# Kernel tuning notes

Hardware: AMD Instinct MI355X
Metric: run time of the kernel (lower is better)

Reference implementation:

```python
import jax, jax.numpy as jnp
import numpy as np

B, S, HID = 1, 2048, 4096
NH, NKV, HD = 32, 8, 128          # num_heads, num_key_value_heads, head_dim
N_REP = NH // NKV                  # GQA group size
ROPE_BASE = 10000.0


def rotate_half(x):
    x1, x2 = jnp.split(x, 2, axis=-1)
    return jnp.concatenate([-x2, x1], axis=-1)


def setup_inputs() -> dict:
    key = jax.random.key(0)
    k_hs, k_q, k_k, k_v, k_o = jax.random.split(key, 5)
    hidden_states = jax.random.normal(k_hs, (B, S, HID), dtype=jnp.float32)
    scale = 0.02
    wq = jax.random.normal(k_q, (HID, NH * HD), dtype=jnp.float32) * scale
    wk = jax.random.normal(k_k, (HID, NKV * HD), dtype=jnp.float32) * scale
    wv = jax.random.normal(k_v, (HID, NKV * HD), dtype=jnp.float32) * scale
    wo = jax.random.normal(k_o, (NH * HD, HID), dtype=jnp.float32) * scale
    # additive causal mask, 0 on/below diagonal, large negative above
    causal = jnp.tril(jnp.ones((S, S), dtype=bool))
    attention_mask = jnp.where(causal, 0.0, -1e9).astype(jnp.float32)[None, None]
    # RoPE cos/sin cache (LlamaRotaryEmbedding)
    inv_freq = 1.0 / (ROPE_BASE ** (jnp.arange(0, HD, 2, dtype=jnp.float32) / HD))
    t = jnp.arange(S, dtype=jnp.float32)
    freqs = jnp.outer(t, inv_freq)                 # [S, HD/2]
    emb = jnp.concatenate([freqs, freqs], axis=-1)  # [S, HD]
    cos, sin = jnp.cos(emb), jnp.sin(emb)
    return {"hidden_states": hidden_states, "attention_mask": attention_mask,
            "wq": wq, "wk": wk, "wv": wv, "wo": wo, "cos": cos, "sin": sin}


def reference(hidden_states, attention_mask, wq, wk, wv, wo, cos, sin):
    b, s, _ = hidden_states.shape
    # projections -> [b, heads, s, head_dim]
    q = (hidden_states @ wq).reshape(b, s, NH, HD).transpose(0, 2, 1, 3)
    k = (hidden_states @ wk).reshape(b, s, NKV, HD).transpose(0, 2, 1, 3)
    v = (hidden_states @ wv).reshape(b, s, NKV, HD).transpose(0, 2, 1, 3)
    # RoPE: cos/sin [s, hd] broadcast over batch and heads
    c = cos[None, None, :, :]
    sn = sin[None, None, :, :]
    q = q * c + rotate_half(q) * sn
    k = k * c + rotate_half(k) * sn
    # GQA repeat_kv: [b, nkv, s, d] -> [b, nh, s, d]
    k = jnp.repeat(k, N_REP, axis=1)
    v = jnp.repeat(v, N_REP, axis=1)
    scores = jnp.einsum('bhqd,bhkd->bhqk', q, k) / jnp.sqrt(jnp.float32(HD))
    scores = scores + attention_mask
    attn = jax.nn.softmax(scores.astype(jnp.float32), axis=-1).astype(q.dtype)
    out = jnp.einsum('bhqk,bhkd->bhqd', attn, v)        # [b, nh, s, d]
    out = out.transpose(0, 2, 1, 3).reshape(b, s, NH * HD)
    return out @ wo
```

## Files before the change

### kernel.cpp

```cpp
#include <hip/hip_runtime.h>


typedef __bf16 bf16_t;
typedef bf16_t bf16x8_t __attribute__((ext_vector_type(8)));
typedef float f32x4_t __attribute__((ext_vector_type(4)));

#define S_LEN 2048
#define HID 4096
#define NH 32
#define NKV 8
#define HD 128
#define KV_DIM 1024
#define QKV_DIM 6144
#define SCALE 0.08838834764831845f

__device__ __align__(16) bf16_t g_hsb[(size_t)S_LEN * HID];
__device__ __align__(16) bf16_t g_wqkvT[(size_t)QKV_DIM * HID];
__device__ __align__(16) bf16_t g_woT[(size_t)HID * HID];
__device__ __align__(16) bf16_t g_qkv[(size_t)S_LEN * QKV_DIM];
__device__ __align__(16) bf16_t g_vT[(size_t)NKV * HD * S_LEN];
__device__ __align__(16) bf16_t g_ao[(size_t)S_LEN * HID];

__device__ __forceinline__ void gl_lds16(const bf16_t* g, bf16_t* l) {
  __builtin_amdgcn_global_load_lds(
      (const __attribute__((address_space(1))) void*)g,
      (__attribute__((address_space(3))) void*)l, 16, 0, 0);
}

__global__ __launch_bounds__(256) void cast_f32_bf16(
    const float* __restrict__ in, bf16_t* __restrict__ out)
{
  size_t i = ((size_t)blockIdx.x * 256 + threadIdx.x) * 8;
  float4 a = *(const float4*)(in + i);
  float4 b = *(const float4*)(in + i + 4);
  bf16x8_t r;
  r[0] = (bf16_t)a.x; r[1] = (bf16_t)a.y; r[2] = (bf16_t)a.z; r[3] = (bf16_t)a.w;
  r[4] = (bf16_t)b.x; r[5] = (bf16_t)b.y; r[6] = (bf16_t)b.z; r[7] = (bf16_t)b.w;
  *(bf16x8_t*)(out + i) = r;
}

__global__ __launch_bounds__(256) void transpose_f32_bf16(
    const float* __restrict__ in, bf16_t* __restrict__ out, int is, int os)
{
  __shared__ __align__(16) bf16_t T[64 * 72];
  int r0 = blockIdx.x * 64, c0 = blockIdx.y * 64;
  int t = threadIdx.x;
#pragma unroll
  for (int it = 0; it < 2; ++it) {
    int idx = t + it * 256;
    int r = idx >> 3, c8 = (idx & 7) * 8;
    const float* p = in + (size_t)(r0 + r) * is + c0 + c8;
    float4 a = *(const float4*)p;
    float4 b = *(const float4*)(p + 4);
    bf16x8_t x;
    x[0] = (bf16_t)a.x; x[1] = (bf16_t)a.y; x[2] = (bf16_t)a.z; x[3] = (bf16_t)a.w;
    x[4] = (bf16_t)b.x; x[5] = (bf16_t)b.y; x[6] = (bf16_t)b.z; x[7] = (bf16_t)b.w;
    *(bf16x8_t*)(T + r * 72 + c8) = x;
  }
  __syncthreads();
#pragma unroll
  for (int it = 0; it < 2; ++it) {
    int idx = t + it * 256;
    int c = idx >> 3, r8 = (idx & 7) * 8;
    bf16x8_t x;
#pragma unroll
    for (int i = 0; i < 8; ++i) x[i] = T[(r8 + i) * 72 + c];
    *(bf16x8_t*)(out + (size_t)(c0 + c) * os + r0 + r8) = x;
  }
}

__global__ __launch_bounds__(256) void transpose_bf16(
    const bf16_t* __restrict__ in, bf16_t* __restrict__ out,
    int is, int os, int in_b, int out_b)
{
  __shared__ __align__(16) bf16_t T[64 * 72];
  const bf16_t* inp = in + (size_t)blockIdx.z * in_b;
  bf16_t* outp = out + (size_t)blockIdx.z * out_b;
  int r0 = blockIdx.x * 64, c0 = blockIdx.y * 64;
  int t = threadIdx.x;
#pragma unroll
  for (int it = 0; it < 2; ++it) {
    int idx = t + it * 256;
    int r = idx >> 3, c8 = (idx & 7) * 8;
    *(bf16x8_t*)(T + r * 72 + c8) =
        *(const bf16x8_t*)(inp + (size_t)(r0 + r) * is + c0 + c8);
  }
  __syncthreads();
#pragma unroll
  for (int it = 0; it < 2; ++it) {
    int idx = t + it * 256;
    int c = idx >> 3, r8 = (idx & 7) * 8;
    bf16x8_t x;
#pragma unroll
    for (int i = 0; i < 8; ++i) x[i] = T[(r8 + i) * 72 + c];
    *(bf16x8_t*)(outp + (size_t)(c0 + c) * os + r0 + r8) = x;
  }
}

template <typename CT>
__global__ __launch_bounds__(256) void gemm128(
    const bf16_t* __restrict__ A, const bf16_t* __restrict__ Bt,
    CT* __restrict__ C, int K, int N)
{
  __shared__ __align__(16) bf16_t As[128 * 32];
  __shared__ __align__(16) bf16_t Bs[128 * 32];
  int t = threadIdx.x;
  int wave = t >> 6, lane = t & 63, ln = lane & 15, lq = lane >> 4;
  int m0 = blockIdx.x * 128, n0 = blockIdx.y * 128;
  int wm = (wave >> 1) * 64, wn = (wave & 1) * 64;
  int srow = wave * 16 + (lane >> 2);
  int skc = (lane & 3) * 8;
  const bf16_t* Ag0 = A + (size_t)(m0 + srow) * K + skc;
  const bf16_t* Ag1 = A + (size_t)(m0 + 64 + srow) * K + skc;
  const bf16_t* Bg0 = Bt + (size_t)(n0 + srow) * K + skc;
  const bf16_t* Bg1 = Bt + (size_t)(n0 + 64 + srow) * K + skc;
  bf16_t* Al0 = As + (wave * 16) * 32;
  bf16_t* Al1 = As + (64 + wave * 16) * 32;
  bf16_t* Bl0 = Bs + (wave * 16) * 32;
  bf16_t* Bl1 = Bs + (64 + wave * 16) * 32;
  f32x4_t acc[4][4] = {};
  for (int k0 = 0; k0 < K; k0 += 32) {
    __syncthreads();
    gl_lds16(Ag0 + k0, Al0);
    gl_lds16(Ag1 + k0, Al1);
    gl_lds16(Bg0 + k0, Bl0);
    gl_lds16(Bg1 + k0, Bl1);
    __syncthreads();
    bf16x8_t af[4], bfr[4];
#pragma unroll
    for (int i = 0; i < 4; ++i) {
      af[i]  = *(const bf16x8_t*)(As + (wm + i * 16 + ln) * 32 + lq * 8);
      bfr[i] = *(const bf16x8_t*)(Bs + (wn + i * 16 + ln) * 32 + lq * 8);
    }
#pragma unroll
    for (int mt = 0; mt < 4; ++mt)
#pragma unroll
      for (int nt = 0; nt < 4; ++nt)
        acc[mt][nt] = __builtin_amdgcn_mfma_f32_16x16x32_bf16(
            af[mt], bfr[nt], acc[mt][nt], 0, 0, 0);
  }
#pragma unroll
  for (int mt = 0; mt < 4; ++mt)
#pragma unroll
    for (int nt = 0; nt < 4; ++nt)
#pragma unroll
      for (int r = 0; r < 4; ++r)
        C[(size_t)(m0 + wm + mt * 16 + lq * 4 + r) * N + n0 + wn + nt * 16 + ln] =
            (CT)acc[mt][nt][r];
}

__global__ __launch_bounds__(256) void rope_kernel(
    bf16_t* __restrict__ qkv, const float* __restrict__ cs,
    const float* __restrict__ sn)
{
  int idx = blockIdx.x * 256 + threadIdx.x;
  int d = idx & 63;
  int h = (idx >> 6) % (NH + NKV);
  int s = idx / (64 * (NH + NKV));
  float c = cs[s * HD + d], si = sn[s * HD + d];
  bf16_t* base = qkv + (size_t)s * QKV_DIM +
                 ((h < NH) ? h * HD : HID + (h - NH) * HD);
  float x1 = (float)base[d], x2 = (float)base[d + 64];
  base[d]      = (bf16_t)(x1 * c - x2 * si);
  base[d + 64] = (bf16_t)(x2 * c + x1 * si);
}

__global__ __launch_bounds__(256) void attn_kernel(
    const bf16_t* __restrict__ QKV, const bf16_t* __restrict__ VT,
    bf16_t* __restrict__ O)
{
  __shared__ __align__(16) bf16_t Ks[64 * 136];
  __shared__ __align__(16) bf16_t Vs[128 * 72];
  __shared__ __align__(16) bf16_t Ps[4 * 16 * 72];
  int t = threadIdx.x, wave = t >> 6, lane = t & 63;
  int ln = lane & 15, lq = lane >> 4;
  int bid = blockIdx.x;
  int qb = (S_LEN / 64 - 1) - (bid >> 5);
  int head = bid & 31, kvh = head >> 2;
  int q0 = qb * 64;
  int qr = q0 + wave * 16 + ln;

  bf16x8_t qf[4];
#pragma unroll
  for (int kk = 0; kk < 4; ++kk)
    qf[kk] = *(const bf16x8_t*)(QKV + (size_t)qr * QKV_DIM + head * HD +
                                kk * 32 + lq * 8);

  f32x4_t oa[8] = {};
  float m_r[4] = {-1e30f, -1e30f, -1e30f, -1e30f};
  float l_r[4] = {0.f, 0.f, 0.f, 0.f};

  int krow = t >> 4, kdc = (t & 15) * 8;
  int vrow = t >> 3, vkc = (t & 7) * 8;
  const bf16_t* Kg = QKV + HID + (size_t)kvh * HD;
  const bf16_t* Vg = VT + (size_t)kvh * HD * S_LEN;

  for (int kt = 0; kt <= qb; ++kt) {
    int kb = kt * 64;
    __syncthreads();
#pragma unroll
    for (int p = 0; p < 4; ++p) {
      int r_ = p * 16 + krow;
      *(bf16x8_t*)(Ks + r_ * 136 + kdc) =
          *(const bf16x8_t*)(Kg + (size_t)(kb + r_) * QKV_DIM + kdc);
      int d_ = p * 32 + vrow;
      *(bf16x8_t*)(Vs + d_ * 72 + vkc) =
          *(const bf16x8_t*)(Vg + (size_t)d_ * S_LEN + kb + vkc);
    }
    __syncthreads();

    f32x4_t sv[4] = {};
#pragma unroll
    for (int nt = 0; nt < 4; ++nt)
#pragma unroll
      for (int kk = 0; kk < 4; ++kk) {
        bf16x8_t kf = *(const bf16x8_t*)(Ks + (nt * 16 + ln) * 136 +
                                         kk * 32 + lq * 8);
        sv[nt] = __builtin_amdgcn_mfma_f32_16x16x32_bf16(qf[kk], kf, sv[nt],
                                                         0, 0, 0);
      }

    float p_[4][4];
    if (kt == qb) {
#pragma unroll
      for (int nt = 0; nt < 4; ++nt)
#pragma unroll
        for (int r = 0; r < 4; ++r) {
          int rq = wave * 16 + lq * 4 + r;
          p_[nt][r] = (nt * 16 + ln <= rq) ? sv[nt][r] * SCALE : -1e30f;
        }
    } else {
#pragma unroll
      for (int nt = 0; nt < 4; ++nt)
#pragma unroll
        for (int r = 0; r < 4; ++r) p_[nt][r] = sv[nt][r] * SCALE;
    }

    float mx[4];
#pragma unroll
    for (int r = 0; r < 4; ++r)
      mx[r] = fmaxf(fmaxf(p_[0][r], p_[1][r]), fmaxf(p_[2][r], p_[3][r]));
#pragma unroll
    for (int off = 8; off >= 1; off >>= 1)
#pragma unroll
      for (int r = 0; r < 4; ++r) mx[r] = fmaxf(mx[r], __shfl_xor(mx[r], off, 64));

    float al[4], rs[4];
#pragma unroll
    for (int r = 0; r < 4; ++r) {
      float mn = fmaxf(m_r[r], mx[r]);
      al[r] = __expf(m_r[r] - mn);
      m_r[r] = mn;
      rs[r] = 0.f;
#pragma unroll
      for (int nt = 0; nt < 4; ++nt) {
        p_[nt][r] = __expf(p_[nt][r] - mn);
        rs[r] += p_[nt][r];
      }
    }
#pragma unroll
    for (int off = 8; off >= 1; off >>= 1)
#pragma unroll
      for (int r = 0; r < 4; ++r) rs[r] += __shfl_xor(rs[r], off, 64);
#pragma unroll
    for (int r = 0; r < 4; ++r) l_r[r] = l_r[r] * al[r] + rs[r];
#pragma unroll
    for (int dt = 0; dt < 8; ++dt)
#pragma unroll
      for (int r = 0; r < 4; ++r) oa[dt][r] *= al[r];

    bf16_t* myP = Ps + wave * 16 * 72;
#pragma unroll
    for (int nt = 0; nt < 4; ++nt)
#pragma unroll
      for (int r = 0; r < 4; ++r)
        myP[(lq * 4 + r) * 72 + nt * 16 + ln] = (bf16_t)p_[nt][r];
    bf16x8_t pf0 = *(const bf16x8_t*)(myP + ln * 72 + lq * 8);
    bf16x8_t pf1 = *(const bf16x8_t*)(myP + ln * 72 + 32 + lq * 8);
#pragma unroll
    for (int dt = 0; dt < 8; ++dt) {
      bf16x8_t v0 = *(const bf16x8_t*)(Vs + (dt * 16 + ln) * 72 + lq * 8);
      bf16x8_t v1 = *(const bf16x8_t*)(Vs + (dt * 16 + ln) * 72 + 32 + lq * 8);
      oa[dt] = __builtin_amdgcn_mfma_f32_16x16x32_bf16(pf0, v0, oa[dt], 0, 0, 0);
      oa[dt] = __builtin_amdgcn_mfma_f32_16x16x32_bf16(pf1, v1, oa[dt], 0, 0, 0);
    }
  }

#pragma unroll
  for (int dt = 0; dt < 8; ++dt)
#pragma unroll
    for (int r = 0; r < 4; ++r) {
      int row = q0 + wave * 16 + lq * 4 + r;
      O[(size_t)row * HID + head * HD + dt * 16 + ln] =
          (bf16_t)(oa[dt][r] / l_r[r]);
    }
}

extern "C" void kernel_launch(void* const* d_in, const int* in_sizes, int n_in,
                              void* d_out, int out_size, void* d_ws, size_t ws_size,
                              hipStream_t stream)
{
  (void)in_sizes; (void)n_in; (void)out_size; (void)d_ws; (void)ws_size;
  const float* hs = (const float*)d_in[0];
  const float* wq = (const float*)d_in[2];
  const float* wk = (const float*)d_in[3];
  const float* wv = (const float*)d_in[4];
  const float* wo = (const float*)d_in[5];
  const float* cs = (const float*)d_in[6];
  const float* sn = (const float*)d_in[7];
  float* out = (float*)d_out;

  bf16_t *hsb, *wqkvT, *woT, *qkv, *vT, *ao;
  hipGetSymbolAddress((void**)&hsb,   HIP_SYMBOL(g_hsb));
  hipGetSymbolAddress((void**)&wqkvT, HIP_SYMBOL(g_wqkvT));
  hipGetSymbolAddress((void**)&woT,   HIP_SYMBOL(g_woT));
  hipGetSymbolAddress((void**)&qkv,   HIP_SYMBOL(g_qkv));
  hipGetSymbolAddress((void**)&vT,    HIP_SYMBOL(g_vT));
  hipGetSymbolAddress((void**)&ao,    HIP_SYMBOL(g_ao));

  cast_f32_bf16<<<(S_LEN * HID) / (256 * 8), 256, 0, stream>>>(hs, hsb);

  transpose_f32_bf16<<<dim3(64, 64), 256, 0, stream>>>(wq, wqkvT, HID, HID);
  transpose_f32_bf16<<<dim3(64, 16), 256, 0, stream>>>(
      wk, wqkvT + (size_t)HID * HID, KV_DIM, HID);
  transpose_f32_bf16<<<dim3(64, 16), 256, 0, stream>>>(
      wv, wqkvT + (size_t)(HID + KV_DIM) * HID, KV_DIM, HID);
  transpose_f32_bf16<<<dim3(64, 64), 256, 0, stream>>>(wo, woT, HID, HID);

  gemm128<bf16_t><<<dim3(S_LEN / 128, QKV_DIM / 128), 256, 0, stream>>>(
      hsb, wqkvT, qkv, HID, QKV_DIM);

  rope_kernel<<<(S_LEN * (NH + NKV) * 64) / 256, 256, 0, stream>>>(qkv, cs, sn);

  transpose_bf16<<<dim3(S_LEN / 64, HD / 64, NKV), 256, 0, stream>>>(
      qkv + HID + KV_DIM, vT, QKV_DIM, S_LEN, HD, HD * S_LEN);

  attn_kernel<<<dim3((S_LEN / 64) * NH), 256, 0, stream>>>(qkv, vT, ao);

  gemm128<float><<<dim3(S_LEN / 128, HID / 128), 256, 0, stream>>>(
      ao, woT, out, HID, HID);
}
```

Baseline: 673.6 us.

## Enlarge attention query tile to 128 rows per block, flatten GEMM grid

The attention kernel now handles 128 query rows per block, two 16-row tiles per wave, so each K/V tile loaded into shared memory serves twice as many queries. This halves K/V reload traffic and the number of barriers per unit of work, at the cost of more registers per thread and half as many blocks. Causal masking is applied to the last two key tiles. The GEMM launches also switch to a 1D grid with explicit m/n decoding, which keeps the same block order (m fastest).

```diff
diff --git a/kernel.cpp b/kernel.cpp
--- a/kernel.cpp
+++ b/kernel.cpp
@@ -100,13 +100,14 @@
 template <typename CT>
 __global__ __launch_bounds__(256) void gemm128(
     const bf16_t* __restrict__ A, const bf16_t* __restrict__ Bt,
-    CT* __restrict__ C, int K, int N)
+    CT* __restrict__ C, int K, int N, int MB)
 {
   __shared__ __align__(16) bf16_t As[128 * 32];
   __shared__ __align__(16) bf16_t Bs[128 * 32];
   int t = threadIdx.x;
   int wave = t >> 6, lane = t & 63, ln = lane & 15, lq = lane >> 4;
-  int m0 = blockIdx.x * 128, n0 = blockIdx.y * 128;
+  int id = blockIdx.x;
+  int m0 = (id % MB) * 128, n0 = (id / MB) * 128;
   int wm = (wave >> 1) * 64, wn = (wave & 1) * 64;
   int srow = wave * 16 + (lane >> 2);
   int skc = (lane & 3) * 8;
@@ -171,31 +172,37 @@
 {
   __shared__ __align__(16) bf16_t Ks[64 * 136];
   __shared__ __align__(16) bf16_t Vs[128 * 72];
-  __shared__ __align__(16) bf16_t Ps[4 * 16 * 72];
+  __shared__ __align__(16) bf16_t Ps[4 * 32 * 72];
   int t = threadIdx.x, wave = t >> 6, lane = t & 63;
   int ln = lane & 15, lq = lane >> 4;
   int bid = blockIdx.x;
-  int qb = (S_LEN / 64 - 1) - (bid >> 5);
+  int qblk = (S_LEN / 128 - 1) - (bid >> 5);
   int head = bid & 31, kvh = head >> 2;
-  int q0 = qb * 64;
-  int qr = q0 + wave * 16 + ln;
-
-  bf16x8_t qf[4];
-#pragma unroll
-  for (int kk = 0; kk < 4; ++kk)
-    qf[kk] = *(const bf16x8_t*)(QKV + (size_t)qr * QKV_DIM + head * HD +
-                                kk * 32 + lq * 8);
-
-  f32x4_t oa[8] = {};
-  float m_r[4] = {-1e30f, -1e30f, -1e30f, -1e30f};
-  float l_r[4] = {0.f, 0.f, 0.f, 0.f};
+  int q0 = qblk * 128;
+
+  bf16x8_t qf[2][4];
+#pragma unroll
+  for (int rt = 0; rt < 2; ++rt)
+#pragma unroll
+    for (int kk = 0; kk < 4; ++kk)
+      qf[rt][kk] = *(const bf16x8_t*)(
+          QKV + (size_t)(q0 + wave * 32 + rt * 16 + ln) * QKV_DIM +
+          head * HD + kk * 32 + lq * 8);
+
+  f32x4_t oa[2][8] = {};
+  float m_r[2][4], l_r[2][4];
+#pragma unroll
+  for (int rt = 0; rt < 2; ++rt)
+#pragma unroll
+    for (int r = 0; r < 4; ++r) { m_r[rt][r] = -1e30f; l_r[rt][r] = 0.f; }
 
   int krow = t >> 4, kdc = (t & 15) * 8;
   int vrow = t >> 3, vkc = (t & 7) * 8;
   const bf16_t* Kg = QKV + HID + (size_t)kvh * HD;
   const bf16_t* Vg = VT + (size_t)kvh * HD * S_LEN;
 
-  for (int kt = 0; kt <= qb; ++kt) {
+  int ktend = 2 * qblk + 1;
+  for (int kt = 0; kt <= ktend; ++kt) {
     int kb = kt * 64;
     __syncthreads();
 #pragma unroll
@@ -209,91 +216,114 @@
     }
     __syncthreads();
 
-    f32x4_t sv[4] = {};
+    f32x4_t sv[2][4] = {};
 #pragma unroll
     for (int nt = 0; nt < 4; ++nt)
 #pragma unroll
       for (int kk = 0; kk < 4; ++kk) {
         bf16x8_t kf = *(const bf16x8_t*)(Ks + (nt * 16 + ln) * 136 +
                                          kk * 32 + lq * 8);
-        sv[nt] = __builtin_amdgcn_mfma_f32_16x16x32_bf16(qf[kk], kf, sv[nt],
-                                                         0, 0, 0);
+        sv[0][nt] = __builtin_amdgcn_mfma_f32_16x16x32_bf16(qf[0][kk], kf,
+                                                            sv[0][nt], 0, 0, 0);
+        sv[1][nt] = __builtin_amdgcn_mfma_f32_16x16x32_bf16(qf[1][kk], kf,
+                                                            sv[1][nt], 0, 0, 0);
       }
 
-    float p_[4][4];
-    if (kt == qb) {
+    float p_[2][4][4];
+    if (kt >= 2 * qblk) {
+#pragma unroll
+      for (int rt = 0; rt < 2; ++rt)
+#pragma unroll
+        for (int nt = 0; nt < 4; ++nt)
+#pragma unroll
+          for (int r = 0; r < 4; ++r) {
+            int rowg = q0 + wave * 32 + rt * 16 + lq * 4 + r;
+            int colg = kb + nt * 16 + ln;
+            p_[rt][nt][r] = (colg <= rowg) ? sv[rt][nt][r] * SCALE : -1e30f;
+          }
+    } else {
+#pragma unroll
+      for (int rt = 0; rt < 2; ++rt)
+#pragma unroll
+        for (int nt = 0; nt < 4; ++nt)
+#pragma unroll
+          for (int r = 0; r < 4; ++r) p_[rt][nt][r] = sv[rt][nt][r] * SCALE;
+    }
+
+#pragma unroll
+    for (int rt = 0; rt < 2; ++rt) {
+      float mx[4], al[4], rs[4];
+#pragma unroll
+      for (int r = 0; r < 4; ++r)
+        mx[r] = fmaxf(fmaxf(p_[rt][0][r], p_[rt][1][r]),
+                      fmaxf(p_[rt][2][r], p_[rt][3][r]));
+#pragma unroll
+      for (int off = 8; off >= 1; off >>= 1)
+#pragma unroll
+        for (int r = 0; r < 4; ++r)
+          mx[r] = fmaxf(mx[r], __shfl_xor(mx[r], off, 64));
+#pragma unroll
+      for (int r = 0; r < 4; ++r) {
+        float mn = fmaxf(m_r[rt][r], mx[r]);
+        al[r] = __expf(m_r[rt][r] - mn);
+        m_r[rt][r] = mn;
+        rs[r] = 0.f;
+#pragma unroll
+        for (int nt = 0; nt < 4; ++nt) {
+          p_[rt][nt][r] = __expf(p_[rt][nt][r] - mn);
+          rs[r] += p_[rt][nt][r];
+        }
+      }
+#pragma unroll
+      for (int off = 8; off >= 1; off >>= 1)
+#pragma unroll
+        for (int r = 0; r < 4; ++r) rs[r] += __shfl_xor(rs[r], off, 64);
+#pragma unroll
+      for (int r = 0; r < 4; ++r) l_r[rt][r] = l_r[rt][r] * al[r] + rs[r];
+#pragma unroll
+      for (int dt = 0; dt < 8; ++dt)
+#pragma unroll
+        for (int r = 0; r < 4; ++r) oa[rt][dt][r] *= al[r];
+    }
+
+    bf16_t* myP = Ps + wave * 32 * 72;
+#pragma unroll
+    for (int rt = 0; rt < 2; ++rt)
 #pragma unroll
       for (int nt = 0; nt < 4; ++nt)
 #pragma unroll
-        for (int r = 0; r < 4; ++r) {
-          int rq = wave * 16 + lq * 4 + r;
-          p_[nt][r] = (nt * 16 + ln <= rq) ? sv[nt][r] * SCALE : -1e30f;
-        }
-    } else {
-#pragma unroll
-      for (int nt = 0; nt < 4; ++nt)
-#pragma unroll
-        for (int r = 0; r < 4; ++r) p_[nt][r] = sv[nt][r] * SCALE;
-    }
-
-    float mx[4];
-#pragma unroll
-    for (int r = 0; r < 4; ++r)
-      mx[r] = fmaxf(fmaxf(p_[0][r], p_[1][r]), fmaxf(p_[2][r], p_[3][r]));
-#pragma unroll
-    for (int off = 8; off >= 1; off >>= 1)
-#pragma unroll
-      for (int r = 0; r < 4; ++r) mx[r] = fmaxf(mx[r], __shfl_xor(mx[r], off, 64));
-
-    float al[4], rs[4];
-#pragma unroll
-    for (int r = 0; r < 4; ++r) {
-      float mn = fmaxf(m_r[r], mx[r]);
-      al[r] = __expf(m_r[r] - mn);
-      m_r[r] = mn;
-      rs[r] = 0.f;
-#pragma unroll
-      for (int nt = 0; nt < 4; ++nt) {
-        p_[nt][r] = __expf(p_[nt][r] - mn);
-        rs[r] += p_[nt][r];
-      }
-    }
-#pragma unroll
-    for (int off = 8; off >= 1; off >>= 1)
-#pragma unroll
-      for (int r = 0; r < 4; ++r) rs[r] += __shfl_xor(rs[r], off, 64);
-#pragma unroll
-    for (int r = 0; r < 4; ++r) l_r[r] = l_r[r] * al[r] + rs[r];
-#pragma unroll
-    for (int dt = 0; dt < 8; ++dt)
-#pragma unroll
-      for (int r = 0; r < 4; ++r) oa[dt][r] *= al[r];
-
-    bf16_t* myP = Ps + wave * 16 * 72;
-#pragma unroll
-    for (int nt = 0; nt < 4; ++nt)
-#pragma unroll
-      for (int r = 0; r < 4; ++r)
-        myP[(lq * 4 + r) * 72 + nt * 16 + ln] = (bf16_t)p_[nt][r];
-    bf16x8_t pf0 = *(const bf16x8_t*)(myP + ln * 72 + lq * 8);
-    bf16x8_t pf1 = *(const bf16x8_t*)(myP + ln * 72 + 32 + lq * 8);
+        for (int r = 0; r < 4; ++r)
+          myP[(rt * 16 + lq * 4 + r) * 72 + nt * 16 + ln] = (bf16_t)p_[rt][nt][r];
+    bf16x8_t pf[2][2];
+#pragma unroll
+    for (int rt = 0; rt < 2; ++rt) {
+      pf[rt][0] = *(const bf16x8_t*)(myP + (rt * 16 + ln) * 72 + lq * 8);
+      pf[rt][1] = *(const bf16x8_t*)(myP + (rt * 16 + ln) * 72 + 32 + lq * 8);
+    }
 #pragma unroll
     for (int dt = 0; dt < 8; ++dt) {
       bf16x8_t v0 = *(const bf16x8_t*)(Vs + (dt * 16 + ln) * 72 + lq * 8);
       bf16x8_t v1 = *(const bf16x8_t*)(Vs + (dt * 16 + ln) * 72 + 32 + lq * 8);
-      oa[dt] = __builtin_amdgcn_mfma_f32_16x16x32_bf16(pf0, v0, oa[dt], 0, 0, 0);
-      oa[dt] = __builtin_amdgcn_mfma_f32_16x16x32_bf16(pf1, v1, oa[dt], 0, 0, 0);
-    }
-  }
-
-#pragma unroll
-  for (int dt = 0; dt < 8; ++dt)
-#pragma unroll
-    for (int r = 0; r < 4; ++r) {
-      int row = q0 + wave * 16 + lq * 4 + r;
-      O[(size_t)row * HID + head * HD + dt * 16 + ln] =
-          (bf16_t)(oa[dt][r] / l_r[r]);
-    }
+#pragma unroll
+      for (int rt = 0; rt < 2; ++rt) {
+        oa[rt][dt] = __builtin_amdgcn_mfma_f32_16x16x32_bf16(pf[rt][0], v0,
+                                                             oa[rt][dt], 0, 0, 0);
+        oa[rt][dt] = __builtin_amdgcn_mfma_f32_16x16x32_bf16(pf[rt][1], v1,
+                                                             oa[rt][dt], 0, 0, 0);
+      }
+    }
+  }
+
+#pragma unroll
+  for (int rt = 0; rt < 2; ++rt)
+#pragma unroll
+    for (int dt = 0; dt < 8; ++dt)
+#pragma unroll
+      for (int r = 0; r < 4; ++r) {
+        int row = q0 + wave * 32 + rt * 16 + lq * 4 + r;
+        O[(size_t)row * HID + head * HD + dt * 16 + ln] =
+            (bf16_t)(oa[rt][dt][r] / l_r[rt][r]);
+      }
 }
 
 extern "C" void kernel_launch(void* const* d_in, const int* in_sizes, int n_in,
@@ -327,16 +357,16 @@
       wv, wqkvT + (size_t)(HID + KV_DIM) * HID, KV_DIM, HID);
   transpose_f32_bf16<<<dim3(64, 64), 256, 0, stream>>>(wo, woT, HID, HID);
 
-  gemm128<bf16_t><<<dim3(S_LEN / 128, QKV_DIM / 128), 256, 0, stream>>>(
-      hsb, wqkvT, qkv, HID, QKV_DIM);
+  gemm128<bf16_t><<<dim3((S_LEN / 128) * (QKV_DIM / 128)), 256, 0, stream>>>(
+      hsb, wqkvT, qkv, HID, QKV_DIM, S_LEN / 128);
 
   rope_kernel<<<(S_LEN * (NH + NKV) * 64) / 256, 256, 0, stream>>>(qkv, cs, sn);
 
   transpose_bf16<<<dim3(S_LEN / 64, HD / 64, NKV), 256, 0, stream>>>(
       qkv + HID + KV_DIM, vT, QKV_DIM, S_LEN, HD, HD * S_LEN);
 
-  attn_kernel<<<dim3((S_LEN / 64) * NH), 256, 0, stream>>>(qkv, vT, ao);
-
-  gemm128<float><<<dim3(S_LEN / 128, HID / 128), 256, 0, stream>>>(
-      ao, woT, out, HID, HID);
-}
+  attn_kernel<<<dim3((S_LEN / 128) * NH), 256, 0, stream>>>(qkv, vT, ao);
+
+  gemm128<float><<<dim3((S_LEN / 128) * (HID / 128)), 256, 0, stream>>>(
+      ao, woT, out, HID, HID, S_LEN / 128);
+}
```

After: 689.2 us. 1.02x slower.
